# Optimization experiments

Hardware: AMD Instinct MI355X
Metric: run time of the kernel (lower is better)

## Reference

```python
import jax, jax.numpy as jnp
import numpy as np

B, S, D, H = 4, 1024, 2048, 16
DK = D // H
SPARSITY = 0.3


def setup_inputs() -> dict:
    key = jax.random.key(0)
    ks = jax.random.split(key, 9)
    scale = 0.02
    return {
        "x": jax.random.normal(ks[0], (B, S, D), dtype=jnp.float32),
        "Wq": jax.random.normal(ks[1], (D, D), dtype=jnp.float32) * scale,
        "bq": jnp.zeros((D,), dtype=jnp.float32),
        "Wk": jax.random.normal(ks[2], (D, D), dtype=jnp.float32) * scale,
        "bk": jnp.zeros((D,), dtype=jnp.float32),
        "Wv": jax.random.normal(ks[3], (D, D), dtype=jnp.float32) * scale,
        "bv": jnp.zeros((D,), dtype=jnp.float32),
        "Wo": jax.random.normal(ks[4], (D, D), dtype=jnp.float32) * scale,
        "bo": jnp.zeros((D,), dtype=jnp.float32),
    }


def reference(x, Wq, bq, Wk, bk, Wv, bv, Wo, bo):
    b, s, d = x.shape
    h, dk = H, d // H
    # projections (torch Linear: x @ W.T + b), split heads -> [b,h,s,dk]
    q = (x @ Wq.T + bq).reshape(b, s, h, dk).transpose(0, 2, 1, 3)
    k = (x @ Wk.T + bk).reshape(b, s, h, dk).transpose(0, 2, 1, 3)
    v = (x @ Wv.T + bv).reshape(b, s, h, dk).transpose(0, 2, 1, 3)
    scores = jnp.einsum("bhqd,bhkd->bhqk", q, k) / jnp.sqrt(jnp.float32(dk))
    kk = max(1, int(s * SPARSITY))
    top_vals, top_idx = jax.lax.top_k(scores, kk)  # [b,h,s,kk]
    # scatter top-k scores into -inf background (matches torch scatter_ on full_like(-inf))
    sparse = jnp.put_along_axis(
        jnp.full_like(scores, -jnp.inf), top_idx, top_vals, axis=-1, inplace=False
    )
    attn = jax.nn.softmax(sparse, axis=-1)  # each row has kk finite entries
    out = jnp.einsum("bhqk,bhkd->bhqd", attn, v)
    out = out.transpose(0, 2, 1, 3).reshape(b, s, d)
    out = out @ Wo.T + bo
    return out, attn
```

## Files before the change

kernel.cpp:

```cpp
#include <hip/hip_runtime.h>
#include <math.h>

#define BB 4
#define SS 1024
#define DD 2048
#define HH 16
#define DKK 128
#define KKTOP 307
#define MROWS (BB * SS)
#define KPLANE ((size_t)MROWS * DD)
static __device__ __constant__ float SCALE = 0.08838834764831845f;

typedef float f32x4 __attribute__((ext_vector_type(4)));
typedef unsigned short su4 __attribute__((ext_vector_type(4)));
typedef unsigned short su8 __attribute__((ext_vector_type(8)));

__device__ __forceinline__ unsigned short f2bf(float x) {
    unsigned u = __float_as_uint(x);
    u += 0x7fffu + ((u >> 16) & 1u);
    return (unsigned short)(u >> 16);
}
__device__ __forceinline__ float bf2f(unsigned short b) {
    return __uint_as_float((unsigned)b << 16);
}
__device__ __forceinline__ unsigned f2u_ord(float f) {
    unsigned x = __float_as_uint(f);
    return (x & 0x80000000u) ? ~x : (x | 0x80000000u);
}
__device__ __forceinline__ float u2f_ord(unsigned u) {
    return __uint_as_float((u & 0x80000000u) ? (u & 0x7fffffffu) : ~u);
}
__device__ __forceinline__ void split4(float4 v, su4& a, su4& b, su4& c) {
    float x[4] = {v.x, v.y, v.z, v.w};
    #pragma unroll
    for (int i = 0; i < 4; ++i) {
        unsigned short b1 = f2bf(x[i]);
        float r = x[i] - bf2f(b1);
        unsigned short b2 = f2bf(r);
        float r2 = r - bf2f(b2);
        a[i] = b1; b[i] = b2; c[i] = f2bf(r2);
    }
}
__device__ __forceinline__ void split2_4(float4 v, su4& a, su4& b) {
    float x[4] = {v.x, v.y, v.z, v.w};
    #pragma unroll
    for (int i = 0; i < 4; ++i) {
        unsigned short b1 = f2bf(x[i]);
        float r = x[i] - bf2f(b1);
        a[i] = b1; b[i] = f2bf(r);
    }
}
__device__ __forceinline__ su8 cat44(su4 a, su4 b) {
    su8 r;
    r[0] = a[0]; r[1] = a[1]; r[2] = a[2]; r[3] = a[3];
    r[4] = b[0]; r[5] = b[1]; r[6] = b[2]; r[7] = b[3];
    return r;
}

#define TM 128
#define TN 128

#define G3LD 40

__global__ __launch_bounds__(256) void gemm_nt_3p(
    const float* __restrict__ A, const float* __restrict__ W,
    const float* __restrict__ bias, float* __restrict__ C,
    int M, int N, int K)
{
    __shared__ unsigned short A1[128][G3LD];
    __shared__ unsigned short A2[128][G3LD];
    __shared__ unsigned short B1[128][G3LD];
    __shared__ unsigned short B2[128][G3LD];

    const int tid = threadIdx.x;
    const int bm = blockIdx.x * 128;
    const int bn = blockIdx.y * 128;
    const int wm = (tid >> 6) & 1;
    const int wn = tid >> 7;
    const int lane = tid & 63;
    const int lrow = tid >> 1;
    const int lcol = (tid & 1) * 16;

    f32x4 acc[4][4];
    #pragma unroll
    for (int i = 0; i < 4; ++i)
        #pragma unroll
        for (int j = 0; j < 4; ++j)
            acc[i][j] = (f32x4){0.f, 0.f, 0.f, 0.f};

    for (int kt = 0; kt < K; kt += 32) {
        __syncthreads();
        {
            const float* Ag = A + (size_t)(bm + lrow) * K + kt + lcol;
            const float* Wg = W + (size_t)(bn + lrow) * K + kt + lcol;
            float4 v0, v1; su4 h0, l0, h1, l1;
            v0 = *(const float4*)(Ag + 0);  v1 = *(const float4*)(Ag + 4);
            split2_4(v0, h0, l0); split2_4(v1, h1, l1);
            *(su8*)&A1[lrow][lcol + 0] = cat44(h0, h1);
            *(su8*)&A2[lrow][lcol + 0] = cat44(l0, l1);
            v0 = *(const float4*)(Ag + 8);  v1 = *(const float4*)(Ag + 12);
            split2_4(v0, h0, l0); split2_4(v1, h1, l1);
            *(su8*)&A1[lrow][lcol + 8] = cat44(h0, h1);
            *(su8*)&A2[lrow][lcol + 8] = cat44(l0, l1);
            v0 = *(const float4*)(Wg + 0);  v1 = *(const float4*)(Wg + 4);
            split2_4(v0, h0, l0); split2_4(v1, h1, l1);
            *(su8*)&B1[lrow][lcol + 0] = cat44(h0, h1);
            *(su8*)&B2[lrow][lcol + 0] = cat44(l0, l1);
            v0 = *(const float4*)(Wg + 8);  v1 = *(const float4*)(Wg + 12);
            split2_4(v0, h0, l0); split2_4(v1, h1, l1);
            *(su8*)&B1[lrow][lcol + 8] = cat44(h0, h1);
            *(su8*)&B2[lrow][lcol + 8] = cat44(l0, l1);
        }
        __syncthreads();

        su8 a1[4], a2[4], b1[4], b2[4];
        #pragma unroll
        for (int f = 0; f < 4; ++f) {
            const int fr = f * 16 + (lane & 15);
            const int fk = (lane >> 4) * 8;
            a1[f] = *(const su8*)&A1[wm * 64 + fr][fk];
            a2[f] = *(const su8*)&A2[wm * 64 + fr][fk];
            b1[f] = *(const su8*)&B1[wn * 64 + fr][fk];
            b2[f] = *(const su8*)&B2[wn * 64 + fr][fk];
        }
        #pragma unroll
        for (int fi = 0; fi < 4; ++fi)
            #pragma unroll
            for (int fj = 0; fj < 4; ++fj) {
                asm volatile("v_mfma_f32_16x16x32_bf16 %0, %1, %2, %0"
                             : "+v"(acc[fi][fj]) : "v"(a1[fi]), "v"(b2[fj]));
                asm volatile("v_mfma_f32_16x16x32_bf16 %0, %1, %2, %0"
                             : "+v"(acc[fi][fj]) : "v"(a2[fi]), "v"(b1[fj]));
                asm volatile("v_mfma_f32_16x16x32_bf16 %0, %1, %2, %0"
                             : "+v"(acc[fi][fj]) : "v"(a1[fi]), "v"(b1[fj]));
            }
    }

    asm volatile("s_nop 7\n\ts_nop 7" ::: "memory");

    #pragma unroll
    for (int fj = 0; fj < 4; ++fj) {
        const int col = bn + wn * 64 + fj * 16 + (lane & 15);
        const float bv = bias[col];
        #pragma unroll
        for (int fi = 0; fi < 4; ++fi) {
            const int r0 = bm + wm * 64 + fi * 16 + (lane >> 4) * 4;
            #pragma unroll
            for (int j = 0; j < 4; ++j)
                C[(size_t)(r0 + j) * N + col] = acc[fi][fj][j] + bv;
        }
    }
}

__global__ __launch_bounds__(256) void gemm_nt_3p_ksplit(
    const float* __restrict__ A, const float* __restrict__ W,
    const float* __restrict__ bias, unsigned short* __restrict__ Ks,
    int M, int N, int K)
{
    __shared__ unsigned short A1[128][G3LD];
    __shared__ unsigned short A2[128][G3LD];
    __shared__ unsigned short B1[128][G3LD];
    __shared__ unsigned short B2[128][G3LD];

    const int tid = threadIdx.x;
    const int bm = blockIdx.x * 128;
    const int bn = blockIdx.y * 128;
    const int wm = (tid >> 6) & 1;
    const int wn = tid >> 7;
    const int lane = tid & 63;
    const int lrow = tid >> 1;
    const int lcol = (tid & 1) * 16;

    f32x4 acc[4][4];
    #pragma unroll
    for (int i = 0; i < 4; ++i)
        #pragma unroll
        for (int j = 0; j < 4; ++j)
            acc[i][j] = (f32x4){0.f, 0.f, 0.f, 0.f};

    for (int kt = 0; kt < K; kt += 32) {
        __syncthreads();
        {
            const float* Ag = A + (size_t)(bm + lrow) * K + kt + lcol;
            const float* Wg = W + (size_t)(bn + lrow) * K + kt + lcol;
            float4 v0, v1; su4 h0, l0, h1, l1;
            v0 = *(const float4*)(Ag + 0);  v1 = *(const float4*)(Ag + 4);
            split2_4(v0, h0, l0); split2_4(v1, h1, l1);
            *(su8*)&A1[lrow][lcol + 0] = cat44(h0, h1);
            *(su8*)&A2[lrow][lcol + 0] = cat44(l0, l1);
            v0 = *(const float4*)(Ag + 8);  v1 = *(const float4*)(Ag + 12);
            split2_4(v0, h0, l0); split2_4(v1, h1, l1);
            *(su8*)&A1[lrow][lcol + 8] = cat44(h0, h1);
            *(su8*)&A2[lrow][lcol + 8] = cat44(l0, l1);
            v0 = *(const float4*)(Wg + 0);  v1 = *(const float4*)(Wg + 4);
            split2_4(v0, h0, l0); split2_4(v1, h1, l1);
            *(su8*)&B1[lrow][lcol + 0] = cat44(h0, h1);
            *(su8*)&B2[lrow][lcol + 0] = cat44(l0, l1);
            v0 = *(const float4*)(Wg + 8);  v1 = *(const float4*)(Wg + 12);
            split2_4(v0, h0, l0); split2_4(v1, h1, l1);
            *(su8*)&B1[lrow][lcol + 8] = cat44(h0, h1);
            *(su8*)&B2[lrow][lcol + 8] = cat44(l0, l1);
        }
        __syncthreads();

        su8 a1[4], a2[4], b1[4], b2[4];
        #pragma unroll
        for (int f = 0; f < 4; ++f) {
            const int fr = f * 16 + (lane & 15);
            const int fk = (lane >> 4) * 8;
            a1[f] = *(const su8*)&A1[wm * 64 + fr][fk];
            a2[f] = *(const su8*)&A2[wm * 64 + fr][fk];
            b1[f] = *(const su8*)&B1[wn * 64 + fr][fk];
            b2[f] = *(const su8*)&B2[wn * 64 + fr][fk];
        }
        #pragma unroll
        for (int fi = 0; fi < 4; ++fi)
            #pragma unroll
            for (int fj = 0; fj < 4; ++fj) {
                asm volatile("v_mfma_f32_16x16x32_bf16 %0, %1, %2, %0"
                             : "+v"(acc[fi][fj]) : "v"(a1[fi]), "v"(b2[fj]));
                asm volatile("v_mfma_f32_16x16x32_bf16 %0, %1, %2, %0"
                             : "+v"(acc[fi][fj]) : "v"(a2[fi]), "v"(b1[fj]));
                asm volatile("v_mfma_f32_16x16x32_bf16 %0, %1, %2, %0"
                             : "+v"(acc[fi][fj]) : "v"(a1[fi]), "v"(b1[fj]));
            }
    }

    asm volatile("s_nop 7\n\ts_nop 7" ::: "memory");

    #pragma unroll
    for (int fj = 0; fj < 4; ++fj) {
        const int col = bn + wn * 64 + fj * 16 + (lane & 15);
        const int h = col >> 7, d = col & (DKK - 1);
        const float bv = bias[col];
        #pragma unroll
        for (int fi = 0; fi < 4; ++fi) {
            const int r0 = bm + wm * 64 + fi * 16 + (lane >> 4) * 4;
            #pragma unroll
            for (int j = 0; j < 4; ++j) {
                const int tok = r0 + j;
                const float val = acc[fi][fj][j] + bv;
                const size_t o = ((size_t)((tok >> 10) * HH + h) * SS
                                  + (tok & (SS - 1))) * DKK + d;
                unsigned short s1 = f2bf(val);
                float r = val - bf2f(s1);
                unsigned short s2 = f2bf(r);
                float r2 = r - bf2f(s2);
                Ks[0 * KPLANE + o] = s1;
                Ks[1 * KPLANE + o] = s2;
                Ks[2 * KPLANE + o] = f2bf(r2);
            }
        }
    }
}

#define GLDA 40

__device__ __forceinline__ su8 pack8(float4 x, float4 y) {
    su8 r;
    r[0] = f2bf(x.x); r[1] = f2bf(x.y); r[2] = f2bf(x.z); r[3] = f2bf(x.w);
    r[4] = f2bf(y.x); r[5] = f2bf(y.y); r[6] = f2bf(y.z); r[7] = f2bf(y.w);
    return r;
}

__global__ __launch_bounds__(256) void gemm_nt_bf16(
    const float* __restrict__ A, const float* __restrict__ W,
    const float* __restrict__ bias, float* __restrict__ C,
    int M, int N, int K)
{
    __shared__ unsigned short Ab[128][GLDA];
    __shared__ unsigned short Bb[128][GLDA];

    const int tid = threadIdx.x;
    const int bm = blockIdx.x * 128;
    const int bn = blockIdx.y * 128;
    const int wm = (tid >> 6) & 1;
    const int wn = tid >> 7;
    const int lane = tid & 63;
    const int lrow = tid >> 1;
    const int lcol = (tid & 1) * 16;

    f32x4 acc[4][4];
    #pragma unroll
    for (int i = 0; i < 4; ++i)
        #pragma unroll
        for (int j = 0; j < 4; ++j)
            acc[i][j] = (f32x4){0.f, 0.f, 0.f, 0.f};

    for (int kt = 0; kt < K; kt += 32) {
        __syncthreads();
        {
            const float* Ag = A + (size_t)(bm + lrow) * K + kt + lcol;
            const float* Wg = W + (size_t)(bn + lrow) * K + kt + lcol;
            float4 a0 = *(const float4*)(Ag + 0);
            float4 a1 = *(const float4*)(Ag + 4);
            float4 a2 = *(const float4*)(Ag + 8);
            float4 a3 = *(const float4*)(Ag + 12);
            *(su8*)&Ab[lrow][lcol + 0] = pack8(a0, a1);
            *(su8*)&Ab[lrow][lcol + 8] = pack8(a2, a3);
            float4 b0 = *(const float4*)(Wg + 0);
            float4 b1 = *(const float4*)(Wg + 4);
            float4 b2 = *(const float4*)(Wg + 8);
            float4 b3 = *(const float4*)(Wg + 12);
            *(su8*)&Bb[lrow][lcol + 0] = pack8(b0, b1);
            *(su8*)&Bb[lrow][lcol + 8] = pack8(b2, b3);
        }
        __syncthreads();

        su8 af[4], bf[4];
        #pragma unroll
        for (int f = 0; f < 4; ++f) {
            af[f] = *(const su8*)&Ab[wm * 64 + f * 16 + (lane & 15)][(lane >> 4) * 8];
            bf[f] = *(const su8*)&Bb[wn * 64 + f * 16 + (lane & 15)][(lane >> 4) * 8];
        }
        #pragma unroll
        for (int fi = 0; fi < 4; ++fi)
            #pragma unroll
            for (int fj = 0; fj < 4; ++fj)
                asm volatile("v_mfma_f32_16x16x32_bf16 %0, %1, %2, %0"
                             : "+v"(acc[fi][fj])
                             : "v"(af[fi]), "v"(bf[fj]));
    }

    asm volatile("s_nop 7\n\ts_nop 7" ::: "memory");

    #pragma unroll
    for (int fj = 0; fj < 4; ++fj) {
        const int col = bn + wn * 64 + fj * 16 + (lane & 15);
        const float bv = bias[col];
        #pragma unroll
        for (int fi = 0; fi < 4; ++fi) {
            const int r0 = bm + wm * 64 + fi * 16 + (lane >> 4) * 4;
            #pragma unroll
            for (int j = 0; j < 4; ++j)
                C[(size_t)(r0 + j) * N + col] = acc[fi][fj][j] + bv;
        }
    }
}

__global__ __launch_bounds__(256) void gemm_nt_bf16_tv(
    const float* __restrict__ A, const float* __restrict__ W,
    const float* __restrict__ bias, unsigned short* __restrict__ Cb,
    int M, int N, int K)
{
    __shared__ unsigned short Ab[128][GLDA];
    __shared__ unsigned short Bb[128][GLDA];

    const int tid = threadIdx.x;
    const int bm = blockIdx.x * 128;
    const int bn = blockIdx.y * 128;
    const int wm = (tid >> 6) & 1;
    const int wn = tid >> 7;
    const int lane = tid & 63;
    const int lrow = tid >> 1;
    const int lcol = (tid & 1) * 16;

    f32x4 acc[4][4];
    #pragma unroll
    for (int i = 0; i < 4; ++i)
        #pragma unroll
        for (int j = 0; j < 4; ++j)
            acc[i][j] = (f32x4){0.f, 0.f, 0.f, 0.f};

    for (int kt = 0; kt < K; kt += 32) {
        __syncthreads();
        {
            const float* Ag = A + (size_t)(bm + lrow) * K + kt + lcol;
            const float* Wg = W + (size_t)(bn + lrow) * K + kt + lcol;
            float4 a0 = *(const float4*)(Ag + 0);
            float4 a1 = *(const float4*)(Ag + 4);
            float4 a2 = *(const float4*)(Ag + 8);
            float4 a3 = *(const float4*)(Ag + 12);
            *(su8*)&Ab[lrow][lcol + 0] = pack8(a0, a1);
            *(su8*)&Ab[lrow][lcol + 8] = pack8(a2, a3);
            float4 b0 = *(const float4*)(Wg + 0);
            float4 b1 = *(const float4*)(Wg + 4);
            float4 b2 = *(const float4*)(Wg + 8);
            float4 b3 = *(const float4*)(Wg + 12);
            *(su8*)&Bb[lrow][lcol + 0] = pack8(b0, b1);
            *(su8*)&Bb[lrow][lcol + 8] = pack8(b2, b3);
        }
        __syncthreads();

        su8 af[4], bf[4];
        #pragma unroll
        for (int f = 0; f < 4; ++f) {
            af[f] = *(const su8*)&Ab[wm * 64 + f * 16 + (lane & 15)][(lane >> 4) * 8];
            bf[f] = *(const su8*)&Bb[wn * 64 + f * 16 + (lane & 15)][(lane >> 4) * 8];
        }
        #pragma unroll
        for (int fi = 0; fi < 4; ++fi)
            #pragma unroll
            for (int fj = 0; fj < 4; ++fj)
                asm volatile("v_mfma_f32_16x16x32_bf16 %0, %1, %2, %0"
                             : "+v"(acc[fi][fj])
                             : "v"(af[fi]), "v"(bf[fj]));
    }

    asm volatile("s_nop 7\n\ts_nop 7" ::: "memory");

    #pragma unroll
    for (int fj = 0; fj < 4; ++fj) {
        const int col = bn + wn * 64 + fj * 16 + (lane & 15);
        #pragma unroll
        for (int fi = 0; fi < 4; ++fi) {
            const int r0 = bm + wm * 64 + fi * 16 + (lane >> 4) * 4;
            #pragma unroll
            for (int j = 0; j < 4; ++j) {
                float v = acc[fi][fj][j] + bias[r0 + j];
                Cb[(size_t)(r0 + j) * N + col] = f2bf(v);
            }
        }
    }
}

#define ATT_LDS 65280

__global__ __launch_bounds__(512) void attn_topk_fused(
    const float* __restrict__ Qb, const unsigned short* __restrict__ Ks,
    const unsigned short* __restrict__ Vt, float* __restrict__ attn_out,
    float* __restrict__ CTX)
{
    __shared__ __align__(16) char smem[ATT_LDS];
    unsigned short* q_s = (unsigned short*)smem;
    unsigned short* k_s = (unsigned short*)(smem + 13056);
    float*          red = (float*)smem;
    unsigned short* wt  = (unsigned short*)(smem + 13056);
    unsigned short* vt  = (unsigned short*)(smem + 13056 + 33024);

    const int tid = threadIdx.x;
    const int wv = tid >> 6, lane = tid & 63;
    const int fg = lane >> 4, fc = lane & 15;

    const int gg = (blockIdx.x & 7) * 512 + ((int)blockIdx.x >> 3);
    const int bh = gg >> 6, qb = gg & 63;
    const int b = bh >> 4, h = bh & 15;
    const int q0 = qb * 16;

    const float* Qg = Qb + (size_t)(b * SS + q0) * DD + h * DKK;
    const unsigned short* Ksg = Ks + (size_t)bh * SS * DKK;
    const unsigned short* Vtg = Vt + (size_t)(h * DKK) * MROWS + b * SS;
    float* aob = attn_out + (size_t)(bh * SS + q0) * SS;

    su8 rk[6];
    #pragma unroll
    for (int pu = 0; pu < 6; ++pu) {
        const int p = pu >> 1;
        const int rem = tid + 512 * (pu & 1);
        const int row = rem >> 4, c8 = rem & 15;
        rk[pu] = *(const su8*)(Ksg + p * KPLANE +
                               (size_t)row * DKK + c8 * 8);
    }

    {
        int row = tid >> 5, c4 = tid & 31;
        float4 v = *(const float4*)(Qg + (size_t)row * DD + c4 * 4);
        int off = row * 136 + c4 * 4;
        su4 p1, p2, p3; split4(v, p1, p2, p3);
        *(su4*)&q_s[off] = p1;
        *(su4*)&q_s[2176 + off] = p2;
        *(su4*)&q_s[4352 + off] = p3;
    }
    __syncthreads();

    const int kt0 = (wv >> 2) * 2;
    su8 af[3][2];
    #pragma unroll
    for (int p = 0; p < 3; ++p)
        #pragma unroll
        for (int kk = 0; kk < 2; ++kk)
            af[p][kk] = *(const su8*)&q_s[p * 2176 + fc * 136 +
                            ((kt0 + kk) * 4 + fg) * 8];

    for (int t = 0; t < 16; ++t) {
        #pragma unroll
        for (int pu = 0; pu < 6; ++pu) {
            const int p = pu >> 1;
            const int rem = tid + 512 * (pu & 1);
            const int row = rem >> 4, c8 = rem & 15;
            *(su8*)&k_s[p * 8704 + row * 136 + c8 * 8] = rk[pu];
        }
        if (t < 15) {
            #pragma unroll
            for (int pu = 0; pu < 6; ++pu) {
                const int p = pu >> 1;
                const int rem = tid + 512 * (pu & 1);
                const int row = rem >> 4, c8 = rem & 15;
                rk[pu] = *(const su8*)(Ksg + p * KPLANE +
                            (size_t)((t + 1) * 64 + row) * DKK + c8 * 8);
            }
        }
        __syncthreads();

        const int krow = (wv & 3) * 16 + fc;
        su8 bf[3][2];
        #pragma unroll
        for (int p = 0; p < 3; ++p)
            #pragma unroll
            for (int kk = 0; kk < 2; ++kk)
                bf[p][kk] = *(const su8*)&k_s[p * 8704 + krow * 136 +
                                ((kt0 + kk) * 4 + fg) * 8];

        f32x4 acc = {0.f, 0.f, 0.f, 0.f};
        constexpr int PI[6] = {2, 0, 1, 1, 0, 0};
        constexpr int PJ[6] = {0, 2, 1, 0, 1, 0};
        #pragma unroll
        for (int p = 0; p < 6; ++p)
            #pragma unroll
            for (int kk = 0; kk < 2; ++kk)
                asm volatile("v_mfma_f32_16x16x32_bf16 %0, %1, %2, %0"
                             : "+v"(acc) : "v"(af[PI[p]][kk]), "v"(bf[PJ[p]][kk]));
        asm volatile("s_nop 7\n\ts_nop 7" ::: "memory");

        if (kt0 == 2) {
            #pragma unroll
            for (int j = 0; j < 4; ++j)
                red[(wv & 3) * 256 + (4 * fg + j) * 16 + fc] = acc[j];
        }
        __syncthreads();
        if (kt0 == 0) {
            #pragma unroll
            for (int j = 0; j < 4; ++j) {
                float s = (acc[j] + red[(wv & 3) * 256 + (4 * fg + j) * 16 + fc]) * SCALE;
                aob[(size_t)(4 * fg + j) * SS + t * 64 + (wv & 3) * 16 + fc] = s;
            }
        }
    }
    __syncthreads();

    unsigned uv[2][16];
    #pragma unroll
    for (int rr = 0; rr < 2; ++rr) {
        const float* aor = aob + (size_t)(2 * wv + rr) * SS;
        #pragma unroll
        for (int t = 0; t < 16; ++t)
            uv[rr][t] = f2u_ord(aor[t * 64 + lane]);
    }
    unsigned pref[2]; int ecnt[2]; float mrow[2], invz[2], tvexp[2];
    #pragma unroll
    for (int rr = 0; rr < 2; ++rr) {
        unsigned p = 0;
        for (int bit = 31; bit >= 0; --bit) {
            unsigned cand = p | (1u << bit);
            int cnt = 0;
            #pragma unroll
            for (int t = 0; t < 16; ++t)
                cnt += __popcll(__ballot(uv[rr][t] >= cand));
            if (cnt >= KKTOP) p = cand;
        }
        pref[rr] = p;
        int g = 0;
        #pragma unroll
        for (int t = 0; t < 16; ++t)
            g += __popcll(__ballot(uv[rr][t] > p));
        ecnt[rr] = KKTOP - g;

        unsigned um = 0;
        #pragma unroll
        for (int t = 0; t < 16; ++t) um = um > uv[rr][t] ? um : uv[rr][t];
        #pragma unroll
        for (int o = 32; o > 0; o >>= 1) {
            unsigned tv2 = __shfl_down(um, o);
            um = um > tv2 ? um : tv2;
        }
        um = __shfl(um, 0);
        const float m = u2f_ord(um);

        float se = 0.f;
        #pragma unroll
        for (int t = 0; t < 16; ++t)
            if (uv[rr][t] > p) se += expf(u2f_ord(uv[rr][t]) - m);
        #pragma unroll
        for (int o = 32; o > 0; o >>= 1) se += __shfl_down(se, o);
        se = __shfl(se, 0);

        mrow[rr] = m;
        tvexp[rr] = expf(u2f_ord(p) - m);
        invz[rr] = 1.0f / (se + (float)ecnt[rr] * tvexp[rr]);
    }

    #pragma unroll
    for (int rr = 0; rr < 2; ++rr) {
        float* aor = aob + (size_t)(2 * wv + rr) * SS;
        unsigned short* wr = wt + (2 * wv + rr) * 1032;
        int tiesbefore = 0;
        #pragma unroll
        for (int t = 0; t < 16; ++t) {
            const unsigned u = uv[rr][t];
            const bool eq = (u == pref[rr]);
            unsigned long long mask = __ballot(eq);
            float w;
            if (u > pref[rr]) {
                w = expf(u2f_ord(u) - mrow[rr]) * invz[rr];
            } else if (eq) {
                int rank = tiesbefore + __popcll(mask & ((1ull << lane) - 1ull));
                w = (rank < ecnt[rr]) ? tvexp[rr] * invz[rr] : 0.f;
            } else {
                w = 0.f;
            }
            aor[t * 64 + lane] = w;
            wr[t * 64 + lane] = f2bf(w);
            tiesbefore += __popcll(mask);
        }
    }

    f32x4 pacc = {0.f, 0.f, 0.f, 0.f};
    const int pvd = wv * 16 + fc;
    su8 rv[2];
    #pragma unroll
    for (int u = 0; u < 2; ++u) {
        int rem = tid + 512 * u;
        int d = rem >> 3, kc = rem & 7;
        rv[u] = *(const su8*)(Vtg + (size_t)d * MROWS + kc * 8);
    }
    for (int t = 0; t < 16; ++t) {
        __syncthreads();
        #pragma unroll
        for (int u = 0; u < 2; ++u) {
            int rem = tid + 512 * u;
            int d = rem >> 3, kc = rem & 7;
            *(su8*)&vt[d * 72 + kc * 8] = rv[u];
        }
        if (t < 15) {
            #pragma unroll
            for (int u = 0; u < 2; ++u) {
                int rem = tid + 512 * u;
                int d = rem >> 3, kc = rem & 7;
                rv[u] = *(const su8*)(Vtg + (size_t)d * MROWS +
                                      (t + 1) * 64 + kc * 8);
            }
        }
        __syncthreads();
        #pragma unroll
        for (int kk = 0; kk < 2; ++kk) {
            su8 aw = *(const su8*)&wt[fc * 1032 + t * 64 + (kk * 4 + fg) * 8];
            su8 bv2 = *(const su8*)&vt[pvd * 72 + (kk * 4 + fg) * 8];
            asm volatile("v_mfma_f32_16x16x32_bf16 %0, %1, %2, %0"
                         : "+v"(pacc) : "v"(aw), "v"(bv2));
        }
    }
    asm volatile("s_nop 7\n\ts_nop 7" ::: "memory");

    #pragma unroll
    for (int j = 0; j < 4; ++j)
        CTX[(size_t)(b * SS + q0 + 4 * fg + j) * DD + h * DKK + pvd] = pacc[j];
}

extern "C" void kernel_launch(void* const* d_in, const int* in_sizes, int n_in,
                              void* d_out, int out_size, void* d_ws, size_t ws_size,
                              hipStream_t stream)
{
    const float* x  = (const float*)d_in[0];
    const float* Wq = (const float*)d_in[1];
    const float* bq = (const float*)d_in[2];
    const float* Wk = (const float*)d_in[3];
    const float* bk = (const float*)d_in[4];
    const float* Wv = (const float*)d_in[5];
    const float* bv = (const float*)d_in[6];
    const float* Wo = (const float*)d_in[7];
    const float* bo = (const float*)d_in[8];

    float* out      = (float*)d_out;
    float* attn_out = (float*)d_out + (size_t)MROWS * DD;

    float* ws = (float*)d_ws;
    const size_t PLANE = (size_t)MROWS * DD;
    float* Qb = ws;
    unsigned short* Ksp = (unsigned short*)(ws + PLANE);
    float* CTX = ws + PLANE + PLANE * 3 / 2;
    unsigned short* Vtp = (unsigned short*)(ws + PLANE + PLANE * 3 / 2 + PLANE);

    dim3 gb(MROWS / TM, DD / TN);
    gemm_nt_3p<<<gb, 256, 0, stream>>>(x, Wq, bq, Qb, MROWS, DD, DD);
    gemm_nt_3p_ksplit<<<gb, 256, 0, stream>>>(x, Wk, bk, Ksp, MROWS, DD, DD);
    gemm_nt_bf16_tv<<<dim3(DD / TM, MROWS / TN), 256, 0, stream>>>(
        Wv, x, bv, Vtp, DD, MROWS, DD);

    attn_topk_fused<<<dim3(BB * HH * (SS / 16)), 512, 0, stream>>>(
        Qb, Ksp, Vtp, attn_out, CTX);

    gemm_nt_bf16<<<gb, 256, 0, stream>>>(CTX, Wo, bo, out, MROWS, DD, DD);
}
```

Measured before the change: 983.5 us.

## Load Q fragments and third K plane directly into registers, shrink LDS

Q is now read straight from global memory into MFMA A-fragments and split into three bf16 planes in registers, so the Q shared-memory staging and its barrier are gone. The third K bf16 plane is prefetched per lane directly from global memory instead of going through LDS. Shared memory per block drops from 65280 to 51456 bytes, and launch bounds now request 6 waves per SIMD, both aimed at higher occupancy. The cost is more uncoalesced per-lane global loads and more register pressure under the tighter launch bound.

```diff
diff --git a/kernel.cpp b/kernel.cpp
--- a/kernel.cpp
+++ b/kernel.cpp
@@ -414,19 +414,18 @@
     }
 }
 
-#define ATT_LDS 65280
-
-__global__ __launch_bounds__(512) void attn_topk_fused(
+#define ATT_LDS 51456
+
+__global__ __launch_bounds__(512, 6) void attn_topk_fused(
     const float* __restrict__ Qb, const unsigned short* __restrict__ Ks,
     const unsigned short* __restrict__ Vt, float* __restrict__ attn_out,
     float* __restrict__ CTX)
 {
     __shared__ __align__(16) char smem[ATT_LDS];
-    unsigned short* q_s = (unsigned short*)smem;
-    unsigned short* k_s = (unsigned short*)(smem + 13056);
     float*          red = (float*)smem;
-    unsigned short* wt  = (unsigned short*)(smem + 13056);
-    unsigned short* vt  = (unsigned short*)(smem + 13056 + 33024);
+    unsigned short* k_s = (unsigned short*)(smem + 4096);
+    unsigned short* wt  = (unsigned short*)smem;
+    unsigned short* vt  = (unsigned short*)(smem + 33024);
 
     const int tid = threadIdx.x;
     const int wv = tid >> 6, lane = tid & 63;
@@ -442,74 +441,86 @@
     const unsigned short* Vtg = Vt + (size_t)(h * DKK) * MROWS + b * SS;
     float* aob = attn_out + (size_t)(bh * SS + q0) * SS;
 
-    su8 rk[6];
-    #pragma unroll
-    for (int pu = 0; pu < 6; ++pu) {
+    const int kt0 = (wv >> 2) * 2;
+    const int krow = (wv & 3) * 16 + fc;
+
+    su8 rk[4];
+    #pragma unroll
+    for (int pu = 0; pu < 4; ++pu) {
         const int p = pu >> 1;
         const int rem = tid + 512 * (pu & 1);
         const int row = rem >> 4, c8 = rem & 15;
         rk[pu] = *(const su8*)(Ksg + p * KPLANE +
                                (size_t)row * DKK + c8 * 8);
     }
-
-    {
-        int row = tid >> 5, c4 = tid & 31;
-        float4 v = *(const float4*)(Qg + (size_t)row * DD + c4 * 4);
-        int off = row * 136 + c4 * 4;
-        su4 p1, p2, p3; split4(v, p1, p2, p3);
-        *(su4*)&q_s[off] = p1;
-        *(su4*)&q_s[2176 + off] = p2;
-        *(su4*)&q_s[4352 + off] = p3;
-    }
-    __syncthreads();
-
-    const int kt0 = (wv >> 2) * 2;
+    const unsigned short* K3g = Ksg + 2 * KPLANE + (size_t)krow * DKK;
+    const int d0a = (kt0 * 4 + fg) * 8;
+    const int d0b = ((kt0 + 1) * 4 + fg) * 8;
+    su8 k3n0 = *(const su8*)(K3g + d0a);
+    su8 k3n1 = *(const su8*)(K3g + d0b);
+
     su8 af[3][2];
     #pragma unroll
-    for (int p = 0; p < 3; ++p)
-        #pragma unroll
-        for (int kk = 0; kk < 2; ++kk)
-            af[p][kk] = *(const su8*)&q_s[p * 2176 + fc * 136 +
-                            ((kt0 + kk) * 4 + fg) * 8];
+    for (int kk = 0; kk < 2; ++kk) {
+        const int d0 = ((kt0 + kk) * 4 + fg) * 8;
+        float4 f0 = *(const float4*)(Qg + (size_t)fc * DD + d0);
+        float4 f1 = *(const float4*)(Qg + (size_t)fc * DD + d0 + 4);
+        su4 a1, a2, a3, b1, b2, b3;
+        split4(f0, a1, a2, a3);
+        split4(f1, b1, b2, b3);
+        af[0][kk] = cat44(a1, b1);
+        af[1][kk] = cat44(a2, b2);
+        af[2][kk] = cat44(a3, b3);
+    }
+
+    unsigned uv[2][16];
 
     for (int t = 0; t < 16; ++t) {
         #pragma unroll
-        for (int pu = 0; pu < 6; ++pu) {
+        for (int pu = 0; pu < 4; ++pu) {
             const int p = pu >> 1;
             const int rem = tid + 512 * (pu & 1);
             const int row = rem >> 4, c8 = rem & 15;
             *(su8*)&k_s[p * 8704 + row * 136 + c8 * 8] = rk[pu];
         }
+        su8 b20 = k3n0, b21 = k3n1;
         if (t < 15) {
             #pragma unroll
-            for (int pu = 0; pu < 6; ++pu) {
+            for (int pu = 0; pu < 4; ++pu) {
                 const int p = pu >> 1;
                 const int rem = tid + 512 * (pu & 1);
                 const int row = rem >> 4, c8 = rem & 15;
                 rk[pu] = *(const su8*)(Ksg + p * KPLANE +
                             (size_t)((t + 1) * 64 + row) * DKK + c8 * 8);
             }
-        }
-        __syncthreads();
-
-        const int krow = (wv & 3) * 16 + fc;
-        su8 bf[3][2];
-        #pragma unroll
-        for (int p = 0; p < 3; ++p)
-            #pragma unroll
-            for (int kk = 0; kk < 2; ++kk)
-                bf[p][kk] = *(const su8*)&k_s[p * 8704 + krow * 136 +
-                                ((kt0 + kk) * 4 + fg) * 8];
+            k3n0 = *(const su8*)(K3g + (size_t)(t + 1) * 64 * DKK + d0a);
+            k3n1 = *(const su8*)(K3g + (size_t)(t + 1) * 64 * DKK + d0b);
+        }
+        __syncthreads();
+
+        su8 bf0[2], bf1[2];
+        #pragma unroll
+        for (int kk = 0; kk < 2; ++kk) {
+            bf0[kk] = *(const su8*)&k_s[0 * 8704 + krow * 136 +
+                            ((kt0 + kk) * 4 + fg) * 8];
+            bf1[kk] = *(const su8*)&k_s[1 * 8704 + krow * 136 +
+                            ((kt0 + kk) * 4 + fg) * 8];
+        }
 
         f32x4 acc = {0.f, 0.f, 0.f, 0.f};
-        constexpr int PI[6] = {2, 0, 1, 1, 0, 0};
-        constexpr int PJ[6] = {0, 2, 1, 0, 1, 0};
-        #pragma unroll
-        for (int p = 0; p < 6; ++p)
-            #pragma unroll
-            for (int kk = 0; kk < 2; ++kk)
-                asm volatile("v_mfma_f32_16x16x32_bf16 %0, %1, %2, %0"
-                             : "+v"(acc) : "v"(af[PI[p]][kk]), "v"(bf[PJ[p]][kk]));
+        #pragma unroll
+        for (int p = 0; p < 6; ++p) {
+            constexpr int PI[6] = {2, 0, 1, 1, 0, 0};
+            constexpr int PJ[6] = {0, 2, 1, 0, 1, 0};
+            #pragma unroll
+            for (int kk = 0; kk < 2; ++kk) {
+                su8 bsel = (PJ[p] == 0) ? bf0[kk]
+                         : (PJ[p] == 1) ? bf1[kk]
+                         : (kk == 0 ? b20 : b21);
+                asm volatile("v_mfma_f32_16x16x32_bf16 %0, %1, %2, %0"
+                             : "+v"(acc) : "v"(af[PI[p]][kk]), "v"(bsel));
+            }
+        }
         asm volatile("s_nop 7\n\ts_nop 7" ::: "memory");
 
         if (kt0 == 2) {
@@ -528,7 +539,6 @@
     }
     __syncthreads();
 
-    unsigned uv[2][16];
     #pragma unroll
     for (int rr = 0; rr < 2; ++rr) {
         const float* aor = aob + (size_t)(2 * wv + rr) * SS;
```

New measurement: 1.404 ms. 1.43x slower.
